# Kernel tuning notes

Hardware: AMD Instinct MI355X
Metric: run time of the kernel (lower is better)

Reference implementation:

```python
import jax, jax.numpy as jnp
import numpy as np

HIDDEN, N_HEADS, N_KV, HD = 2560, 32, 8, 80
B, S = 2, 2048

def apply_rope(x, cos_f, sin_f):
    # x: [B, S, H, hd]; cos_f/sin_f: [S, hd]
    seq_len = x.shape[1]
    cos = cos_f[:seq_len][None, :, None, :]
    sin = sin_f[:seq_len][None, :, None, :]
    hd = x.shape[-1]
    x1, x2 = x[..., : hd // 2], x[..., hd // 2 :]
    return x * cos + jnp.concatenate([-x2, x1], axis=-1) * sin


def setup_inputs() -> dict:
    key = jax.random.key(0)
    ks = jax.random.split(key, 7)
    sd = 0.02
    return {
        "x": jax.random.normal(ks[0], (B, S, HIDDEN), dtype=jnp.float32),
        "cos_f": jax.random.uniform(ks[1], (S, HD), dtype=jnp.float32),
        "sin_f": jax.random.uniform(ks[2], (S, HD), dtype=jnp.float32),
        "Wq": jax.random.normal(ks[3], (HIDDEN, N_HEADS * HD), dtype=jnp.float32) * sd,
        "Wk": jax.random.normal(ks[4], (HIDDEN, N_KV * HD), dtype=jnp.float32) * sd,
        "Wv": jax.random.normal(ks[5], (HIDDEN, N_KV * HD), dtype=jnp.float32) * sd,
        "Wo": jax.random.normal(ks[6], (N_HEADS * HD, HIDDEN), dtype=jnp.float32) * sd,
    }


def reference(x, cos_f, sin_f, Wq, Wk, Wv, Wo):
    b, s, _ = x.shape
    q = (x @ Wq).reshape(b, s, N_HEADS, HD)
    k = (x @ Wk).reshape(b, s, N_KV, HD)
    v = (x @ Wv).reshape(b, s, N_KV, HD)
    q = apply_rope(q, cos_f, sin_f)
    k = apply_rope(k, cos_f, sin_f)
    g = N_HEADS // N_KV
    k = jnp.repeat(k, g, axis=2)  # [b, s, n_heads, hd]
    v = jnp.repeat(v, g, axis=2)
    q, k, v = [jnp.transpose(t, (0, 2, 1, 3)) for t in (q, k, v)]  # [b, h, s, hd]
    scale = jnp.sqrt(jnp.float32(HD))
    w = jnp.einsum("bhqd,bhkd->bhqk", q, k) / scale
    causal = jnp.triu(jnp.full((s, s), -1e9, dtype=w.dtype), k=1)
    w = w + causal[None, None]
    w = jax.nn.softmax(w.astype(jnp.float32), axis=-1).astype(q.dtype)
    o = jnp.einsum("bhqk,bhkd->bhqd", w, v)
    o = jnp.transpose(o, (0, 2, 1, 3)).reshape(b, s, N_HEADS * HD)
    return o @ Wo
```

## Files before the change

kernel.cpp:

```cpp
#include <hip/hip_runtime.h>
#include <hip/hip_bf16.h>
#include <math.h>

#define HIDDEN 2560
#define NH 32
#define NKV 8
#define HD 80
#define BATCH 2
#define SEQ 2048
#define QH_COLS (NH*HD)
#define KV_COLS (NKV*HD)
#define QKV_COLS (QH_COLS + 2*KV_COLS)
#define ROWS (BATCH*SEQ)

typedef __attribute__((ext_vector_type(4))) float floatx4;
typedef __attribute__((ext_vector_type(16))) float floatx16;
typedef __attribute__((ext_vector_type(8))) short shortx8;
typedef __attribute__((ext_vector_type(4))) unsigned short u16x4;
typedef unsigned short u16;

__device__ inline u16 f2bf(float f) { __hip_bfloat16 h = __float2bfloat16(f); return *(u16*)&h; }
__device__ inline void storeC(float v, float* p) { *p = v; }
__device__ inline void storeC(float v, u16* p) { *p = f2bf(v); }

#if __has_builtin(__builtin_amdgcn_exp2f)
__device__ inline float fexp2(float x) { return __builtin_amdgcn_exp2f(x); }
#else
__device__ inline float fexp2(float x) { return __expf(x * 0.6931471805599453f); }
#endif

__device__ __forceinline__ unsigned cvtpk(float lo, float hi2) {
    unsigned r;
    asm("v_cvt_pk_bf16_f32 %0, %1, %2" : "=v"(r) : "v"(lo), "v"(hi2));
    return r;
}
__device__ __forceinline__ void pl32swap(unsigned &a, unsigned &b) {
#if __has_builtin(__builtin_amdgcn_permlane32_swap)
    auto r = __builtin_amdgcn_permlane32_swap(a, b, false, false);
    a = r[0]; b = r[1];
#else
    asm("v_permlane32_swap_b32 %0, %1" : "+v"(a), "+v"(b));
#endif
}

#define GLL(gp, lp) __builtin_amdgcn_global_load_lds( \
    (const __attribute__((address_space(1))) unsigned int*)(gp), \
    (__attribute__((address_space(3))) unsigned int*)(lp), 16, 0, 0)

__global__ __launch_bounds__(256) void conv_bf16(const float* __restrict__ x,
                                                 u16* __restrict__ y) {
    int i = (blockIdx.x * 256 + threadIdx.x) * 4;
    float4 v = *(const float4*)(x + i);
    u16x4 o = { f2bf(v.x), f2bf(v.y), f2bf(v.z), f2bf(v.w) };
    *(u16x4*)(y + i) = o;
}

__global__ __launch_bounds__(256) void transpose_conv(const float* __restrict__ W,
                                                      u16* __restrict__ Wt,
                                                      int K, int N) {
    __shared__ float tile[64][65];
    const int tid = threadIdx.x;
    const int n0 = blockIdx.x * 64, k0 = blockIdx.y * 64;
    const int r = tid >> 4, c4 = (tid & 15) * 4;
#pragma unroll
    for (int i = 0; i < 4; i++) {
        float4 v = *(const float4*)(W + (size_t)(k0 + r + i * 16) * N + n0 + c4);
        tile[r + i * 16][c4 + 0] = v.x;
        tile[r + i * 16][c4 + 1] = v.y;
        tile[r + i * 16][c4 + 2] = v.z;
        tile[r + i * 16][c4 + 3] = v.w;
    }
    __syncthreads();
    const int n = tid >> 2, kg = (tid & 3) * 16;
    __align__(16) u16 tmp[16];
#pragma unroll
    for (int j = 0; j < 16; j++) tmp[j] = f2bf(tile[kg + j][n]);
    u16* dst = Wt + (size_t)(n0 + n) * K + k0 + kg;
    *(uint4*)dst = *(const uint4*)tmp;
    *(uint4*)(dst + 8) = *(const uint4*)(tmp + 8);
}

#define STAGE_HALF(MP, ROFF, T, KH) do { \
    GLL(MP + (T) * 64 + (KH) * 32 + skc * 8,       SM + (ROFF) + skc * 2048 + srow8); \
    GLL(MP + (T) * 64 + (KH) * 32 + (skc + 2) * 8, SM + (ROFF) + (skc + 2) * 2048 + srow8); \
} while (0)

#define MFMA16(IH) \
    __builtin_amdgcn_s_setprio(1); \
    acc[(IH)*4+0][0] = __builtin_amdgcn_mfma_f32_16x16x32_bf16(a0, b0, acc[(IH)*4+0][0], 0, 0, 0); \
    acc[(IH)*4+0][1] = __builtin_amdgcn_mfma_f32_16x16x32_bf16(a0, b1, acc[(IH)*4+0][1], 0, 0, 0); \
    acc[(IH)*4+0][2] = __builtin_amdgcn_mfma_f32_16x16x32_bf16(a0, b2, acc[(IH)*4+0][2], 0, 0, 0); \
    acc[(IH)*4+0][3] = __builtin_amdgcn_mfma_f32_16x16x32_bf16(a0, b3, acc[(IH)*4+0][3], 0, 0, 0); \
    acc[(IH)*4+1][0] = __builtin_amdgcn_mfma_f32_16x16x32_bf16(a1, b0, acc[(IH)*4+1][0], 0, 0, 0); \
    acc[(IH)*4+1][1] = __builtin_amdgcn_mfma_f32_16x16x32_bf16(a1, b1, acc[(IH)*4+1][1], 0, 0, 0); \
    acc[(IH)*4+1][2] = __builtin_amdgcn_mfma_f32_16x16x32_bf16(a1, b2, acc[(IH)*4+1][2], 0, 0, 0); \
    acc[(IH)*4+1][3] = __builtin_amdgcn_mfma_f32_16x16x32_bf16(a1, b3, acc[(IH)*4+1][3], 0, 0, 0); \
    acc[(IH)*4+2][0] = __builtin_amdgcn_mfma_f32_16x16x32_bf16(a2, b0, acc[(IH)*4+2][0], 0, 0, 0); \
    acc[(IH)*4+2][1] = __builtin_amdgcn_mfma_f32_16x16x32_bf16(a2, b1, acc[(IH)*4+2][1], 0, 0, 0); \
    acc[(IH)*4+2][2] = __builtin_amdgcn_mfma_f32_16x16x32_bf16(a2, b2, acc[(IH)*4+2][2], 0, 0, 0); \
    acc[(IH)*4+2][3] = __builtin_amdgcn_mfma_f32_16x16x32_bf16(a2, b3, acc[(IH)*4+2][3], 0, 0, 0); \
    acc[(IH)*4+3][0] = __builtin_amdgcn_mfma_f32_16x16x32_bf16(a3, b0, acc[(IH)*4+3][0], 0, 0, 0); \
    acc[(IH)*4+3][1] = __builtin_amdgcn_mfma_f32_16x16x32_bf16(a3, b1, acc[(IH)*4+3][1], 0, 0, 0); \
    acc[(IH)*4+3][2] = __builtin_amdgcn_mfma_f32_16x16x32_bf16(a3, b2, acc[(IH)*4+3][2], 0, 0, 0); \
    acc[(IH)*4+3][3] = __builtin_amdgcn_mfma_f32_16x16x32_bf16(a3, b3, acc[(IH)*4+3][3], 0, 0, 0); \
    __builtin_amdgcn_s_setprio(0);

#define PHASE(BUFB, KH, IH, RDB, STAGE_STMT, VM_STMT) { \
    const u16* _ar = SM + (BUFB) + (KH) * 8192 + aoff + (IH) * 512; \
    shortx8 a0 = *(const shortx8*)(_ar); \
    shortx8 a1 = *(const shortx8*)(_ar + 128); \
    shortx8 a2 = *(const shortx8*)(_ar + 256); \
    shortx8 a3 = *(const shortx8*)(_ar + 384); \
    if (RDB) { \
        const u16* _br = SM + (BUFB) + (KH) * 8192 + boff; \
        b0 = *(const shortx8*)(_br); \
        b1 = *(const shortx8*)(_br + 128); \
        b2 = *(const shortx8*)(_br + 256); \
        b3 = *(const shortx8*)(_br + 384); \
    } \
    STAGE_STMT; \
    asm volatile("" ::: "memory"); \
    __builtin_amdgcn_s_barrier(); \
    __builtin_amdgcn_sched_barrier(0); \
    MFMA16(IH); \
    VM_STMT; \
    asm volatile("" ::: "memory"); \
    __builtin_amdgcn_s_barrier(); \
    __builtin_amdgcn_sched_barrier(0); \
}

template <typename OutT>
__global__ __launch_bounds__(512, 2) void gemm256(const u16* __restrict__ A,
                                                  const u16* __restrict__ Bt,
                                                  OutT* __restrict__ C,
                                                  int M, int N, int K,
                                                  int nbx) {
    __shared__ __align__(16) u16 SM[65536];
    const int tid = threadIdx.x;
    const int wave = tid >> 6, lane = tid & 63;
    const int m16 = lane & 15, quad = lane >> 4;
    const int wm = wave >> 2, wn = wave & 3;

    const int nwg = nbx * (M >> 8);
    const int cpx = nwg >> 3;
    const int bid = (int)blockIdx.x;
    const int swzb = (bid & 7) * cpx + (bid >> 3);
    const int bm = (swzb / nbx) * 256, bn = (swzb % nbx) * 256;

    const int srow = tid & 255, skc = tid >> 8;
    const int srow8 = srow * 8;
    const u16* pA = A  + (size_t)(bm + srow) * K;
    const u16* pB = Bt + (size_t)(bn + srow) * K;

    const int aoff = quad * 2048 + (wm * 128 + m16) * 8;
    const int boff = 16384 + quad * 2048 + (wn * 64 + m16) * 8;

    floatx4 acc[8][4];
#pragma unroll
    for (int i = 0; i < 8; i++)
#pragma unroll
        for (int j = 0; j < 4; j++) acc[i][j] = (floatx4){0.f, 0.f, 0.f, 0.f};

    const int nkt = K >> 6;
    const int nit = nkt >> 1;

    STAGE_HALF(pA, 0,     0, 0);
    STAGE_HALF(pB, 16384, 0, 0);
    STAGE_HALF(pA, 8192,  0, 1);
    STAGE_HALF(pB, 24576, 0, 1);
    STAGE_HALF(pA, 32768, 1, 0);
    STAGE_HALF(pB, 49152, 1, 0);
    STAGE_HALF(pA, 40960, 1, 1);
    STAGE_HALF(pB, 57344, 1, 1);
    asm volatile("s_waitcnt vmcnt(8)" ::: "memory");
    __builtin_amdgcn_s_barrier();

    for (int it = 0; it < nit; ++it) {
        const int t0 = 2 * it, t1 = t0 + 1;
        const bool pf = (it + 1 < nit);
        shortx8 b0, b1, b2, b3;
        PHASE(0, 0, 0, true,
              { if (it) STAGE_HALF(pA, 40960, t1, 1); }, {});
        PHASE(0, 0, 1, false,
              { if (pf) STAGE_HALF(pB, 16384, t0 + 2, 0); }, {});
        PHASE(0, 1, 0, true,
              { if (pf) STAGE_HALF(pA, 0, t0 + 2, 0); }, {});
        PHASE(0, 1, 1, false,
              { if (pf) STAGE_HALF(pB, 24576, t0 + 2, 1); },
              { if (pf) { asm volatile("s_waitcnt vmcnt(6)" ::: "memory"); }
                else    { asm volatile("s_waitcnt vmcnt(0)" ::: "memory"); } });
        PHASE(32768, 0, 0, true,
              { if (pf) STAGE_HALF(pA, 8192, t0 + 2, 1); }, {});
        PHASE(32768, 0, 1, false,
              { if (pf) STAGE_HALF(pB, 49152, t1 + 2, 0); }, {});
        PHASE(32768, 1, 0, true,
              { if (pf) STAGE_HALF(pA, 32768, t1 + 2, 0); }, {});
        PHASE(32768, 1, 1, false,
              { if (pf) STAGE_HALF(pB, 57344, t1 + 2, 1); },
              { if (pf) { asm volatile("s_waitcnt vmcnt(6)" ::: "memory"); }
                else    { asm volatile("s_waitcnt vmcnt(0)" ::: "memory"); } });
    }

#pragma unroll
    for (int i = 0; i < 8; i++)
#pragma unroll
        for (int j = 0; j < 4; j++)
#pragma unroll
            for (int p = 0; p < 4; p++) {
                int row = bm + wm * 128 + i * 16 + quad * 4 + p;
                int col = bn + wn * 64 + j * 16 + m16;
                storeC(acc[i][j][p], &C[(size_t)row * N + col]);
            }
}

__global__ __launch_bounds__(256) void rope_bf16(__hip_bfloat16* __restrict__ qkv,
                                                 const float* __restrict__ cf,
                                                 const float* __restrict__ sf) {
    int idx = blockIdx.x * 256 + threadIdx.x;
    int d  = idx % 40;
    int t  = idx / 40;
    int hh = t % (NH + NKV);
    int g  = t / (NH + NKV);
    int s  = g & (SEQ - 1);
    float c1 = cf[s * HD + d],      s1 = sf[s * HD + d];
    float c2 = cf[s * HD + d + 40], s2 = sf[s * HD + d + 40];
    const float qsc = (hh < NH) ? (float)(0.11180339887498949 * 1.4426950408889634) : 1.0f;
    __hip_bfloat16* p = (hh < NH) ? (qkv + (size_t)g * QKV_COLS + hh * HD)
                                  : (qkv + (size_t)g * QKV_COLS + QH_COLS + (hh - NH) * HD);
    float x1 = __bfloat162float(p[d]);
    float x2 = __bfloat162float(p[d + 40]);
    p[d]      = __float2bfloat16((x1 * c1 - x2 * s1) * qsc);
    p[d + 40] = __float2bfloat16((x2 * c2 + x1 * s2) * qsc);
}

__device__ __forceinline__ void stage_K(const u16* kg, u16* dst, int wave, int lane) {
#pragma unroll
    for (int t = 0; t < 2; t++) {
        int s = t * 256 + wave * 64 + lane;
        int db = t * 4 + wave;
        GLL(kg + (size_t)lane * QKV_COLS + db * 8, dst + s * 8);
    }
    if (wave < 2) {
        int s = 512 + wave * 64 + lane;
        int db = 8 + wave;
        GLL(kg + (size_t)lane * QKV_COLS + db * 8, dst + s * 8);
    }
}

__device__ __forceinline__ void load_V(const u16* vg, shortx8* vr, int wave, int lane) {
#pragma unroll
    for (int t = 0; t < 2; t++) {
        int db = t * 4 + wave;
        vr[t] = *(const shortx8*)(vg + (size_t)lane * QKV_COLS + db * 8);
    }
    if (wave < 2) vr[2] = *(const shortx8*)(vg + (size_t)lane * QKV_COLS + (8 + wave) * 8);
}

__device__ __forceinline__ void scatter_V(u16* Vs, const shortx8* vr, int wave, int lane) {
    const int kc = lane >> 3, jj = lane & 7;
    u16* base = Vs + kc * 768 + jj;
#pragma unroll
    for (int t = 0; t < 2; t++) {
        int db = t * 4 + wave;
#pragma unroll
        for (int i = 0; i < 8; i++) base[db * 64 + ((i ^ kc) << 3)] = vr[t][i];
    }
    if (wave < 2) {
        int db = 8 + wave;
#pragma unroll
        for (int i = 0; i < 8; i++) base[db * 64 + ((i ^ kc) << 3)] = vr[2][i];
    }
}

__global__ __launch_bounds__(256, 3) void attn_mfma(const u16* __restrict__ qkv,
                                                    u16* __restrict__ ob) {
    __shared__ __align__(16) u16 SM[16384];
    u16* Kbuf = SM;
    u16* Vs   = SM + 10240;

    const int tid  = threadIdx.x;
    const int wave = tid >> 6;
    const int lane = tid & 63;
    const int l31  = lane & 31;
    const int hi   = lane >> 5;

    const int idx = blockIdx.x;
    const int qt  = 15 - (idx >> 6);
    const int hb  = idx & 63;
    const int h   = hb >> 1;
    const int b   = hb & 1;
    const int kvh = h >> 2;
    const int qb  = qt * 128 + wave * 32;

    const u16* qgb = qkv + (size_t)(b * SEQ + qt * 128) * QKV_COLS + h * HD;
    const u16* kg0 = qkv + (size_t)(b * SEQ) * QKV_COLS + QH_COLS + kvh * HD;
    const u16* vg0 = qkv + (size_t)(b * SEQ) * QKV_COLS + QH_COLS + KV_COLS + kvh * HD;

    {
        int kc = tid >> 5, o = (tid & 31) * 4;
        *(u16x4*)(Vs + kc * 768 + 640 + o) = (u16x4){0, 0, 0, 0};
    }

#pragma unroll
    for (int t = 0; t < 5; t++) {
        int s = t * 256 + tid;
        int row = s / 10, ch = s % 10;
        GLL(qgb + (size_t)row * QKV_COLS + ch * 8, SM + s * 8);
    }
    __syncthreads();
    shortx8 qf[5];
    {
        const u16* qrow = SM + (wave * 32 + l31) * 80 + hi * 8;
#pragma unroll
        for (int c = 0; c < 5; c++) qf[c] = *(const shortx8*)(qrow + c * 16);
    }
    __syncthreads();

    int vbase[4];
#pragma unroll
    for (int c = 0; c < 4; c++) {
        int k8 = c * 2 + hi;
        vbase[c] = k8 * 768 + ((l31 & 24) + ((l31 & 7) ^ k8)) * 8;
    }
    const u16* kfp = Kbuf + hi * 512 + l31 * 8;

    stage_K(kg0, Kbuf, wave, lane);
    shortx8 vr[3];
    load_V(vg0, vr, wave, lane);
    __syncthreads();
    scatter_V(Vs, vr, wave, lane);
    __syncthreads();

    floatx16 Oacc[3];
#pragma unroll
    for (int n = 0; n < 3; n++)
#pragma unroll
        for (int r = 0; r < 16; r++) Oacc[n][r] = 0.0f;
    float mrow = -1.0e30f, lrow = 0.0f;
    int cur = 0;
    const int nkt = 2 * qt + 2;

    for (int kt = 0; kt < nkt; kt++) {
        const bool last = (kt == nkt - 1);
        if (!last) {
            const u16* kg = kg0 + (size_t)(kt + 1) * 64 * QKV_COLS;
            const u16* vg = vg0 + (size_t)(kt + 1) * 64 * QKV_COLS;
            stage_K(kg, Kbuf + (cur ^ 1) * 5120, wave, lane);
            load_V(vg, vr, wave, lane);
        }

        const bool active = (kt * 64 <= qb + 31);
        if (active) {
            const u16* kp = kfp + cur * 5120;
            const bool kr1   = (kt * 64 + 32 <= qb + 31);
            const bool dmask = (kt * 64 + 63 > qb);
            floatx16 S0, S1;
            {
                floatx16 s;
#pragma unroll
                for (int r = 0; r < 16; r++) s[r] = 0.0f;
#pragma unroll
                for (int c = 0; c < 5; c++) {
                    shortx8 kf = *(const shortx8*)(kp + c * 1024);
                    s = __builtin_amdgcn_mfma_f32_32x32x16_bf16(kf, qf[c], s, 0, 0, 0);
                }
                S0 = s;
            }
            if (kr1) {
                floatx16 s;
#pragma unroll
                for (int r = 0; r < 16; r++) s[r] = 0.0f;
#pragma unroll
                for (int c = 0; c < 5; c++) {
                    shortx8 kf = *(const shortx8*)(kp + c * 1024 + 256);
                    s = __builtin_amdgcn_mfma_f32_32x32x16_bf16(kf, qf[c], s, 0, 0, 0);
                }
                S1 = s;
            }
            const int qrel = qb + l31 - kt * 64;
            if (dmask) {
#pragma unroll
                for (int r = 0; r < 16; r++) {
                    int rr = (r & 3) + 8 * (r >> 2) + 4 * hi;
                    if (rr > qrel) S0[r] = -1.0e30f;
                    if (kr1 && (32 + rr) > qrel) S1[r] = -1.0e30f;
                }
            }
            float mx = mrow;
#pragma unroll
            for (int r = 0; r < 16; r++) mx = fmaxf(mx, S0[r]);
            if (kr1) {
#pragma unroll
                for (int r = 0; r < 16; r++) mx = fmaxf(mx, S1[r]);
            }
            mx = fmaxf(mx, __shfl_xor(mx, 32));
            if (!__all(mx - mrow <= 8.0f)) {
                float alpha = fexp2(mrow - mx);
                lrow *= alpha;
#pragma unroll
                for (int n = 0; n < 3; n++)
#pragma unroll
                    for (int r = 0; r < 16; r++) Oacc[n][r] *= alpha;
                mrow = mx;
            }
            float rsum = 0.0f;
#pragma unroll
            for (int r = 0; r < 16; r++) { float p = fexp2(S0[r] - mrow); rsum += p; S0[r] = p; }
            if (kr1) {
#pragma unroll
                for (int r = 0; r < 16; r++) { float p = fexp2(S1[r] - mrow); rsum += p; S1[r] = p; }
            }
            rsum += __shfl_xor(rsum, 32);
            lrow += rsum;

#pragma unroll
            for (int kr = 0; kr < 2; kr++) {
                if (kr == 1 && !kr1) break;
                floatx16& Sv = (kr == 0) ? S0 : S1;
                unsigned d0[4], d1[4];
#pragma unroll
                for (int m = 0; m < 4; m++) {
                    d0[m] = cvtpk(Sv[4 * m + 0], Sv[4 * m + 1]);
                    d1[m] = cvtpk(Sv[4 * m + 2], Sv[4 * m + 3]);
                }
#pragma unroll
                for (int cb = 0; cb < 2; cb++) {
                    int c = kr * 2 + cb;
                    if (kt * 64 + c * 16 > qb + 31) break;
                    unsigned x0 = d0[2 * cb], y0 = d0[2 * cb + 1];
                    unsigned x1 = d1[2 * cb], y1 = d1[2 * cb + 1];
                    pl32swap(x0, y0);
                    pl32swap(x1, y1);
                    union { unsigned u[4]; shortx8 s8; } pf;
                    pf.u[0] = x0; pf.u[1] = x1; pf.u[2] = y0; pf.u[3] = y1;
#pragma unroll
                    for (int n = 0; n < 3; n++) {
                        shortx8 vf = *(const shortx8*)(Vs + vbase[c] + n * 256);
                        Oacc[n] = __builtin_amdgcn_mfma_f32_32x32x16_bf16(vf, pf.s8, Oacc[n], 0, 0, 0);
                    }
                }
            }
        }

        if (last) break;
        __syncthreads();
        scatter_V(Vs, vr, wave, lane);
        cur ^= 1;
        __syncthreads();
    }

    const float invl = 1.0f / lrow;
    u16* op = ob + (size_t)(b * SEQ + qt * 128 + wave * 32 + l31) * QH_COLS + h * HD + 4 * hi;
#pragma unroll
    for (int n = 0; n < 3; n++) {
        const int mmax = (n == 2) ? 2 : 4;
#pragma unroll
        for (int m = 0; m < mmax; m++) {
            u16x4 o4 = { f2bf(Oacc[n][4 * m + 0] * invl), f2bf(Oacc[n][4 * m + 1] * invl),
                         f2bf(Oacc[n][4 * m + 2] * invl), f2bf(Oacc[n][4 * m + 3] * invl) };
            *(u16x4*)(op + n * 32 + 8 * m) = o4;
        }
    }
}

extern "C" void kernel_launch(void* const* d_in, const int* in_sizes, int n_in,
                              void* d_out, int out_size, void* d_ws, size_t ws_size,
                              hipStream_t stream) {
    const float* x    = (const float*)d_in[0];
    const float* cf   = (const float*)d_in[1];
    const float* sf   = (const float*)d_in[2];
    const float* Wq   = (const float*)d_in[3];
    const float* Wk   = (const float*)d_in[4];
    const float* Wv   = (const float*)d_in[5];
    const float* Wo   = (const float*)d_in[6];
    float* out = (float*)d_out;

    u16* xh    = (u16*)d_ws;
    u16* Wqkvt = xh    + (size_t)ROWS * HIDDEN;
    u16* Wot   = Wqkvt + (size_t)QKV_COLS * HIDDEN;
    u16* qkv   = Wot   + (size_t)QH_COLS * HIDDEN;
    u16* obh   = xh;

    dim3 blk(256);
    conv_bf16<<<(ROWS * HIDDEN / 4) / 256, blk, 0, stream>>>(x, xh);
    transpose_conv<<<dim3(QH_COLS / 64, HIDDEN / 64), blk, 0, stream>>>(Wq, Wqkvt, HIDDEN, QH_COLS);
    transpose_conv<<<dim3(KV_COLS / 64, HIDDEN / 64), blk, 0, stream>>>(Wk, Wqkvt + (size_t)QH_COLS * HIDDEN, HIDDEN, KV_COLS);
    transpose_conv<<<dim3(KV_COLS / 64, HIDDEN / 64), blk, 0, stream>>>(Wv, Wqkvt + (size_t)(QH_COLS + KV_COLS) * HIDDEN, HIDDEN, KV_COLS);
    transpose_conv<<<dim3(HIDDEN / 64, QH_COLS / 64), blk, 0, stream>>>(Wo, Wot, QH_COLS, HIDDEN);

    gemm256<u16><<<dim3((QKV_COLS / 256) * (ROWS / 256)), dim3(512), 0, stream>>>(xh, Wqkvt, qkv, ROWS, QKV_COLS, HIDDEN, QKV_COLS / 256);

    rope_bf16<<<(ROWS * (NH + NKV) * 40) / 256, blk, 0, stream>>>((__hip_bfloat16*)qkv, cf, sf);
    attn_mfma<<<dim3(16 * 64), blk, 0, stream>>>(qkv, obh);

    gemm256<float><<<dim3((HIDDEN / 256) * (ROWS / 256)), dim3(512), 0, stream>>>(obh, Wot, out, ROWS, HIDDEN, QH_COLS, HIDDEN / 256);
}
```

Before: 468.0 us.

## Restructure GEMM main loop to one barrier per MFMA phase with finer vmcnt waits

Replaces the PHASE macro, which used two barriers per 16-MFMA phase, with an explicit schedule that has a single barrier per phase. The global-to-LDS staging order is reshuffled: the last prologue stages move into the loop, and vmcnt waits sit between phases. The aim is to halve barrier stalls and overlap LDS reads and global loads more tightly with MFMA work. With one barrier, correctness depends on the new ordering and waitcnt values, which risks LDS write-after-read races.

After: 473.8 us. No clear change (+1.2%).

```diff
diff --git a/kernel.cpp b/kernel.cpp
--- a/kernel.cpp
+++ b/kernel.cpp
@@ -84,6 +84,16 @@
     GLL(MP + (T) * 64 + (KH) * 32 + skc * 8,       SM + (ROFF) + skc * 2048 + srow8); \
     GLL(MP + (T) * 64 + (KH) * 32 + (skc + 2) * 8, SM + (ROFF) + (skc + 2) * 2048 + srow8); \
 } while (0)
+
+#define VMCNT(N) asm volatile("s_waitcnt vmcnt(" #N ")" ::: "memory")
+#define BARSB do { __builtin_amdgcn_s_barrier(); __builtin_amdgcn_sched_barrier(0); } while (0)
+
+#define LOAD_B(BUFB, KH) do { const u16* _br = SM + (BUFB) + (KH) * 8192 + boff; \
+    b0 = *(const shortx8*)(_br);        b1 = *(const shortx8*)(_br + 128); \
+    b2 = *(const shortx8*)(_br + 256);  b3 = *(const shortx8*)(_br + 384); } while (0)
+#define LOAD_A(BUFB, KH, IH) do { const u16* _ar = SM + (BUFB) + (KH) * 8192 + aoff + (IH) * 512; \
+    a0 = *(const shortx8*)(_ar);        a1 = *(const shortx8*)(_ar + 128); \
+    a2 = *(const shortx8*)(_ar + 256);  a3 = *(const shortx8*)(_ar + 384); } while (0)
 
 #define MFMA16(IH) \
     __builtin_amdgcn_s_setprio(1); \
@@ -105,30 +115,6 @@
     acc[(IH)*4+3][3] = __builtin_amdgcn_mfma_f32_16x16x32_bf16(a3, b3, acc[(IH)*4+3][3], 0, 0, 0); \
     __builtin_amdgcn_s_setprio(0);
 
-#define PHASE(BUFB, KH, IH, RDB, STAGE_STMT, VM_STMT) { \
-    const u16* _ar = SM + (BUFB) + (KH) * 8192 + aoff + (IH) * 512; \
-    shortx8 a0 = *(const shortx8*)(_ar); \
-    shortx8 a1 = *(const shortx8*)(_ar + 128); \
-    shortx8 a2 = *(const shortx8*)(_ar + 256); \
-    shortx8 a3 = *(const shortx8*)(_ar + 384); \
-    if (RDB) { \
-        const u16* _br = SM + (BUFB) + (KH) * 8192 + boff; \
-        b0 = *(const shortx8*)(_br); \
-        b1 = *(const shortx8*)(_br + 128); \
-        b2 = *(const shortx8*)(_br + 256); \
-        b3 = *(const shortx8*)(_br + 384); \
-    } \
-    STAGE_STMT; \
-    asm volatile("" ::: "memory"); \
-    __builtin_amdgcn_s_barrier(); \
-    __builtin_amdgcn_sched_barrier(0); \
-    MFMA16(IH); \
-    VM_STMT; \
-    asm volatile("" ::: "memory"); \
-    __builtin_amdgcn_s_barrier(); \
-    __builtin_amdgcn_sched_barrier(0); \
-}
-
 template <typename OutT>
 __global__ __launch_bounds__(512, 2) void gemm256(const u16* __restrict__ A,
                                                   const u16* __restrict__ Bt,
@@ -170,35 +156,39 @@
     STAGE_HALF(pB, 24576, 0, 1);
     STAGE_HALF(pA, 32768, 1, 0);
     STAGE_HALF(pB, 49152, 1, 0);
-    STAGE_HALF(pA, 40960, 1, 1);
-    STAGE_HALF(pB, 57344, 1, 1);
-    asm volatile("s_waitcnt vmcnt(8)" ::: "memory");
+    VMCNT(8);
     __builtin_amdgcn_s_barrier();
+    __builtin_amdgcn_sched_barrier(0);
 
     for (int it = 0; it < nit; ++it) {
         const int t0 = 2 * it, t1 = t0 + 1;
         const bool pf = (it + 1 < nit);
-        shortx8 b0, b1, b2, b3;
-        PHASE(0, 0, 0, true,
-              { if (it) STAGE_HALF(pA, 40960, t1, 1); }, {});
-        PHASE(0, 0, 1, false,
-              { if (pf) STAGE_HALF(pB, 16384, t0 + 2, 0); }, {});
-        PHASE(0, 1, 0, true,
-              { if (pf) STAGE_HALF(pA, 0, t0 + 2, 0); }, {});
-        PHASE(0, 1, 1, false,
-              { if (pf) STAGE_HALF(pB, 24576, t0 + 2, 1); },
-              { if (pf) { asm volatile("s_waitcnt vmcnt(6)" ::: "memory"); }
-                else    { asm volatile("s_waitcnt vmcnt(0)" ::: "memory"); } });
-        PHASE(32768, 0, 0, true,
-              { if (pf) STAGE_HALF(pA, 8192, t0 + 2, 1); }, {});
-        PHASE(32768, 0, 1, false,
-              { if (pf) STAGE_HALF(pB, 49152, t1 + 2, 0); }, {});
-        PHASE(32768, 1, 0, true,
-              { if (pf) STAGE_HALF(pA, 32768, t1 + 2, 0); }, {});
-        PHASE(32768, 1, 1, false,
-              { if (pf) STAGE_HALF(pB, 57344, t1 + 2, 1); },
-              { if (pf) { asm volatile("s_waitcnt vmcnt(6)" ::: "memory"); }
-                else    { asm volatile("s_waitcnt vmcnt(0)" ::: "memory"); } });
+        shortx8 a0, a1, a2, a3, b0, b1, b2, b3;
+        LOAD_A(0, 0, 0); LOAD_B(0, 0);
+        STAGE_HALF(pB, 57344, t1, 1);
+        BARSB; MFMA16(0);
+        LOAD_A(0, 0, 1);
+        STAGE_HALF(pA, 40960, t1, 1);
+        if (pf) { VMCNT(6); } else { VMCNT(8); }
+        BARSB; MFMA16(1);
+        LOAD_A(0, 1, 0); LOAD_B(0, 1);
+        if (pf) STAGE_HALF(pB, 16384, t0 + 2, 0);
+        BARSB; MFMA16(0);
+        LOAD_A(0, 1, 1);
+        if (pf) { STAGE_HALF(pA, 0, t0 + 2, 0); VMCNT(6); } else { VMCNT(4); }
+        BARSB; MFMA16(1);
+        LOAD_A(32768, 0, 0); LOAD_B(32768, 0);
+        if (pf) STAGE_HALF(pB, 24576, t0 + 2, 1);
+        BARSB; MFMA16(0);
+        LOAD_A(32768, 0, 1);
+        if (pf) { STAGE_HALF(pA, 8192, t0 + 2, 1); VMCNT(6); } else { VMCNT(0); }
+        BARSB; MFMA16(1);
+        LOAD_A(32768, 1, 0); LOAD_B(32768, 1);
+        if (pf) STAGE_HALF(pB, 49152, t1 + 2, 0);
+        BARSB; MFMA16(0);
+        LOAD_A(32768, 1, 1);
+        if (pf) { STAGE_HALF(pA, 32768, t1 + 2, 0); VMCNT(6); }
+        BARSB; MFMA16(1);
     }
 
 #pragma unroll
```
